# Kernel tuning notes

Hardware: AMD Instinct MI355X
Metric: run time of the kernel (lower is better)

The kernel has to match this reference:

```python
import jax, jax.numpy as jnp
import numpy as np

B, S, D = 8, 4096, 1536
NUM_ORGANISMS = 4
OUT = 2048


def setup_inputs() -> dict:
    key = jax.random.key(0)
    k_x, k_idx, k_w = jax.random.split(key, 3)
    x = jax.random.normal(k_x, (B, S, D), dtype=jnp.float32)
    organism_index = jax.random.randint(k_idx, (B,), 0, NUM_ORGANISMS, dtype=jnp.int32)
    # TruncatedNormal(stddev=1/sqrt(D)) init; plain normal*stddev is a faithful stand-in
    stddev = 1.0 / np.sqrt(D)
    w = jax.random.normal(k_w, (NUM_ORGANISMS, D, OUT), dtype=jnp.float32) * stddev
    b = jnp.zeros((NUM_ORGANISMS, OUT), dtype=jnp.float32)
    return {"x": x, "organism_index": organism_index, "w": w, "b": b}


def reference(x, organism_index, w, b):
    # Gather per-batch organism weights/biases (hard routing), then batched matmul.
    w_b = w[organism_index]          # [B, D, OUT]
    b_b = b[organism_index]          # [B, OUT]
    out = jnp.einsum('bsi,bij->bsj', x, w_b,
                     preferred_element_type=jnp.float32)  # [B, S, OUT]
    return out + b_b[:, None, :]
```

## Files before the change

kernel.cpp:

```cpp
#include <hip/hip_runtime.h>
#include <hip/hip_bf16.h>
#include <stdint.h>

#define B_    8
#define S_    4096
#define D_    1536
#define ORG_  4
#define OUT_  2048

typedef __bf16 bf16;
typedef __attribute__((ext_vector_type(8))) bf16  bf16x8;
typedef __attribute__((ext_vector_type(4))) float f32x4;

#define BK64 64
#define NKT  (D_ / BK64)

__global__ void k_cvt_x(const float* __restrict__ x, bf16* __restrict__ xb, long n8) {
  long i = (long)blockIdx.x * blockDim.x + threadIdx.x;
  long stride = (long)gridDim.x * blockDim.x;
  for (; i < n8; i += stride) {
    const float4* p = (const float4*)(x + i * 8);
    float4 a = p[0];
    float4 b = p[1];
    bf16x8 v;
    v[0] = (bf16)a.x; v[1] = (bf16)a.y; v[2] = (bf16)a.z; v[3] = (bf16)a.w;
    v[4] = (bf16)b.x; v[5] = (bf16)b.y; v[6] = (bf16)b.z; v[7] = (bf16)b.w;
    *(bf16x8*)(xb + i * 8) = v;
  }
}

__global__ void k_cvt_wT(const float* __restrict__ w, bf16* __restrict__ wt) {
  __shared__ float tile[32][33];
  int org = blockIdx.z;
  int n0 = blockIdx.x * 32;
  int d0 = blockIdx.y * 32;
  const float* wsrc = w + (size_t)org * D_ * OUT_;
  bf16* wdst = wt + (size_t)org * OUT_ * D_;
  int tx = threadIdx.x, ty = threadIdx.y;
#pragma unroll
  for (int j = 0; j < 32; j += 8)
    tile[ty + j][tx] = wsrc[(size_t)(d0 + ty + j) * OUT_ + (n0 + tx)];
  __syncthreads();
#pragma unroll
  for (int j = 0; j < 32; j += 8)
    wdst[(size_t)(n0 + ty + j) * D_ + (d0 + tx)] = (bf16)tile[tx][ty + j];
}

__global__ __launch_bounds__(512, 2)
void k_gemm256(const bf16* __restrict__ xb, const bf16* __restrict__ wt,
               const int* __restrict__ oidx, const float* __restrict__ bias,
               float* __restrict__ out) {
  __shared__ __align__(16) char smem[131072];
  char* const ldsA = smem;
  char* const ldsB = smem + 65536;

  const int batch = blockIdx.y;
  const int bx = blockIdx.x;
  const int swz = (bx & 7) * 16 + (bx >> 3);
  const int tn = swz >> 4, tm = swz & 15;
  const int m0 = tm * 256, n0 = tn * 256;
  const int org = oidx[batch];

  const bf16* Ag = xb + (size_t)batch * S_ * D_ + (size_t)m0 * D_;
  const bf16* Bg = wt + (size_t)org * OUT_ * D_ + (size_t)n0 * D_;

  const int tid  = threadIdx.x;
  const int lane = tid & 63, wv = tid >> 6;
  const int wr = wv >> 2, wc = wv & 3;
  const int lm = lane & 15, lk = lane >> 4;

  const int xo0 = (lk * 16) ^ ((lm & 7) << 4);
  const int xo1 = (64 + lk * 16) ^ ((lm & 7) << 4);
  const int arow = (wr * 128 + lm) * 128;
  const int brow = (wc * 64  + lm) * 128;

  const int srow = tid >> 3;
  const int scol = ((tid & 7) ^ ((tid >> 3) & 7)) << 3;
  const int soff = wv * 1024;

#define LDA(v, mi, kk) (*(const bf16x8*)(ldsA + (v)*32768 + arow + (mi)*2048 + ((kk) ? xo1 : xo0)))
#define LDB(v, ni, kk) (*(const bf16x8*)(ldsB + (v)*32768 + brow + (ni)*2048 + ((kk) ? xo1 : xo0)))

#define STAGE_HALF(gptr, ldsbase, h, kb) do {                                            \
    __builtin_amdgcn_global_load_lds(                                                    \
      (__attribute__((address_space(1))) void*)((gptr) + (size_t)((h)*128 + srow) * D_ + (kb) + scol), \
      (__attribute__((address_space(3))) void*)((ldsbase) + (h)*16384 + soff), 16, 0, 0);\
    __builtin_amdgcn_global_load_lds(                                                    \
      (__attribute__((address_space(1))) void*)((gptr) + (size_t)((h)*128 + 64 + srow) * D_ + (kb) + scol), \
      (__attribute__((address_space(3))) void*)((ldsbase) + (h)*16384 + 8192 + soff), 16, 0, 0); \
  } while (0)

#define SBAR()  __builtin_amdgcn_s_barrier()
#define LGK0()  asm volatile("s_waitcnt lgkmcnt(0)" ::: "memory")
#define VMC4()  asm volatile("s_waitcnt vmcnt(4)" ::: "memory")
#define VMC0()  asm volatile("s_waitcnt vmcnt(0)" ::: "memory")
#define PRIO(p) __builtin_amdgcn_s_setprio(p)

  bf16x8 a[4][2], b0[2][2], b1[2][2];
  f32x4 acc[8][4];
#pragma unroll
  for (int m = 0; m < 8; ++m)
#pragma unroll
    for (int n = 0; n < 4; ++n) acc[m][n] = (f32x4){0.f, 0.f, 0.f, 0.f};

#define READ_A(v, mb) do { _Pragma("unroll") for (int m = 0; m < 4; ++m) { \
    a[m][0] = LDA(v, (mb) + m, 0); a[m][1] = LDA(v, (mb) + m, 1); } } while (0)
#define READ_B(v, nb, bb) do { _Pragma("unroll") for (int n = 0; n < 2; ++n) { \
    bb[n][0] = LDB(v, (nb) + n, 0); bb[n][1] = LDB(v, (nb) + n, 1); } } while (0)
#define MFMA_Q(mb, nb, bb) do { \
    _Pragma("unroll") for (int m = 0; m < 4; ++m) \
    _Pragma("unroll") for (int n = 0; n < 2; ++n) \
    _Pragma("unroll") for (int kk = 0; kk < 2; ++kk) \
      acc[(mb)+m][(nb)+n] = __builtin_amdgcn_mfma_f32_16x16x32_bf16( \
          a[m][kk], bb[n][kk], acc[(mb)+m][(nb)+n], 0, 0, 0); } while (0)

  STAGE_HALF(Bg, ldsB, 0, 0);
  STAGE_HALF(Bg, ldsB, 1, 0);
  STAGE_HALF(Ag, ldsA, 0, 0);
  STAGE_HALF(Ag, ldsA, 1, 0);
  STAGE_HALF(Bg, ldsB + 32768, 0, BK64);
  STAGE_HALF(Bg, ldsB + 32768, 1, BK64);
  VMC4();
  SBAR();

  for (int i = 0; i < NKT / 2; ++i) {
    const int k1 = (2 * i + 1) * BK64;
    int t2 = 2 * i + 2; if (t2 > NKT - 1) t2 = NKT - 1;
    int t3 = 2 * i + 3; if (t3 > NKT - 1) t3 = NKT - 1;
    const int k2 = t2 * BK64, k3 = t3 * BK64;

    READ_A(0, 0); READ_B(0, 0, b0);
    STAGE_HALF(Ag, ldsA + 32768, 0, k1);
    SBAR(); LGK0();
    PRIO(1); MFMA_Q(0, 0, b0); PRIO(0);
    SBAR();
    READ_B(0, 2, b1);
    STAGE_HALF(Ag, ldsA + 32768, 1, k1);
    SBAR(); LGK0();
    PRIO(1); MFMA_Q(0, 2, b1); PRIO(0);
    SBAR();
    READ_A(0, 4);
    STAGE_HALF(Bg, ldsB, 0, k2);
    SBAR(); LGK0();
    PRIO(1); MFMA_Q(4, 0, b0); PRIO(0);
    SBAR();
    STAGE_HALF(Bg, ldsB, 1, k2);
    SBAR();
    PRIO(1); MFMA_Q(4, 2, b1); PRIO(0);
    VMC4();
    SBAR();
    READ_A(1, 0); READ_B(1, 0, b0);
    STAGE_HALF(Ag, ldsA, 0, k2);
    SBAR(); LGK0();
    PRIO(1); MFMA_Q(0, 0, b0); PRIO(0);
    SBAR();
    READ_B(1, 2, b1);
    STAGE_HALF(Ag, ldsA, 1, k2);
    SBAR(); LGK0();
    PRIO(1); MFMA_Q(0, 2, b1); PRIO(0);
    SBAR();
    READ_A(1, 4);
    STAGE_HALF(Bg, ldsB + 32768, 0, k3);
    SBAR(); LGK0();
    PRIO(1); MFMA_Q(4, 0, b0); PRIO(0);
    SBAR();
    STAGE_HALF(Bg, ldsB + 32768, 1, k3);
    SBAR();
    PRIO(1); MFMA_Q(4, 2, b1); PRIO(0);
    VMC4();
    SBAR();
  }

  VMC0();

  float* Og = out + (size_t)batch * S_ * OUT_ + (size_t)m0 * OUT_ + n0;
  const float* bbase = bias + (size_t)org * OUT_ + n0;
#pragma unroll
  for (int n = 0; n < 4; ++n) {
    const int col = wc * 64 + n * 16 + lm;
    const float bv = bbase[col];
#pragma unroll
    for (int m = 0; m < 8; ++m) {
#pragma unroll
      for (int r = 0; r < 4; ++r) {
        const int row = wr * 128 + m * 16 + lk * 4 + r;
        Og[(size_t)row * OUT_ + col] = acc[m][n][r] + bv;
      }
    }
  }
#undef LDA
#undef LDB
#undef STAGE_HALF
#undef SBAR
#undef LGK0
#undef VMC4
#undef VMC0
#undef PRIO
#undef READ_A
#undef READ_B
#undef MFMA_Q
}

__global__ void k_gemm_fallback(const float* __restrict__ x, const int* __restrict__ oidx,
                                const float* __restrict__ w, const float* __restrict__ bias,
                                float* __restrict__ out) {
  const int b = blockIdx.z;
  const int org = oidx[b];
  const int n = blockIdx.x * 64 + threadIdx.x;
  const int m = blockIdx.y * 4 + threadIdx.y;
  const float* xr = x + ((size_t)b * S_ + m) * D_;
  const float* wp = w + (size_t)org * D_ * OUT_ + n;
  float acc = 0.f;
  for (int k = 0; k < D_; ++k) acc += xr[k] * wp[(size_t)k * OUT_];
  out[((size_t)b * S_ + m) * OUT_ + n] = acc + bias[(size_t)org * OUT_ + n];
}

extern "C" void kernel_launch(void* const* d_in, const int* in_sizes, int n_in,
                              void* d_out, int out_size, void* d_ws, size_t ws_size,
                              hipStream_t stream) {
  const float* x    = (const float*)d_in[0];
  const int*   oidx = (const int*)d_in[1];
  const float* w    = (const float*)d_in[2];
  const float* bias = (const float*)d_in[3];
  float* out = (float*)d_out;

  const size_t xb_elems = (size_t)B_ * S_ * D_;
  const size_t wt_elems = (size_t)ORG_ * OUT_ * D_;
  const size_t need = (xb_elems + wt_elems) * sizeof(bf16);

  if (ws_size < need) {
    dim3 g(OUT_ / 64, S_ / 4, B_);
    k_gemm_fallback<<<g, dim3(64, 4), 0, stream>>>(x, oidx, w, bias, out);
    return;
  }

  bf16* xb = (bf16*)d_ws;
  bf16* wt = xb + xb_elems;

  k_cvt_x<<<2048, 256, 0, stream>>>(x, xb, (long)(xb_elems / 8));
  dim3 gt(OUT_ / 32, D_ / 32, ORG_);
  k_cvt_wT<<<gt, dim3(32, 8), 0, stream>>>(w, wt);
  dim3 gg(128, B_);
  k_gemm256<<<gg, 512, 0, stream>>>(xb, wt, oidx, bias, out);
}
```

Baseline: 313.2 us.

## Make GEMM persistent over four tiles with cross-tile prefetch

```diff
diff --git a/kernel.cpp b/kernel.cpp
--- a/kernel.cpp
+++ b/kernel.cpp
@@ -14,6 +14,7 @@
 
 #define BK64 64
 #define NKT  (D_ / BK64)
+#define ROUNDS 4
 
 __global__ void k_cvt_x(const float* __restrict__ x, bf16* __restrict__ xb, long n8) {
   long i = (long)blockIdx.x * blockDim.x + threadIdx.x;
@@ -47,22 +48,30 @@
 }
 
 __global__ __launch_bounds__(512, 2)
-void k_gemm256(const bf16* __restrict__ xb, const bf16* __restrict__ wt,
-               const int* __restrict__ oidx, const float* __restrict__ bias,
-               float* __restrict__ out) {
+void k_gemm_pers(const bf16* __restrict__ xb, const bf16* __restrict__ wt,
+                 const int* __restrict__ oidx, const float* __restrict__ bias,
+                 float* __restrict__ out) {
   __shared__ __align__(16) char smem[131072];
   char* const ldsA = smem;
   char* const ldsB = smem + 65536;
 
-  const int batch = blockIdx.y;
   const int bx = blockIdx.x;
-  const int swz = (bx & 7) * 16 + (bx >> 3);
-  const int tn = swz >> 4, tm = swz & 15;
-  const int m0 = tm * 256, n0 = tn * 256;
-  const int org = oidx[batch];
-
-  const bf16* Ag = xb + (size_t)batch * S_ * D_ + (size_t)m0 * D_;
-  const bf16* Bg = wt + (size_t)org * OUT_ * D_ + (size_t)n0 * D_;
+  const int gbase = (bx & 7) * 32 + (bx >> 3);
+
+  const bf16* AgR[ROUNDS]; const bf16* BgR[ROUNDS];
+  float* OgR[ROUNDS]; const float* bbR[ROUNDS];
+#pragma unroll
+  for (int r = 0; r < ROUNDS; ++r) {
+    const int G = gbase + r * 256;
+    const int pair = G >> 4, tm = G & 15;
+    const int batch = pair >> 3, tn = pair & 7;
+    const int m0 = tm * 256, n0 = tn * 256;
+    const int org = oidx[batch];
+    AgR[r] = xb + (size_t)batch * S_ * D_ + (size_t)m0 * D_;
+    BgR[r] = wt + (size_t)org * OUT_ * D_ + (size_t)n0 * D_;
+    OgR[r] = out + (size_t)batch * S_ * OUT_ + (size_t)m0 * OUT_ + n0;
+    bbR[r] = bias + (size_t)org * OUT_ + n0;
+  }
 
   const int tid  = threadIdx.x;
   const int lane = tid & 63, wv = tid >> 6;
@@ -92,6 +101,7 @@
 
 #define SBAR()  __builtin_amdgcn_s_barrier()
 #define LGK0()  asm volatile("s_waitcnt lgkmcnt(0)" ::: "memory")
+#define LGK8()  asm volatile("s_waitcnt lgkmcnt(8)" ::: "memory")
 #define VMC4()  asm volatile("s_waitcnt vmcnt(4)" ::: "memory")
 #define VMC0()  asm volatile("s_waitcnt vmcnt(0)" ::: "memory")
 #define PRIO(p) __builtin_amdgcn_s_setprio(p)
@@ -114,91 +124,108 @@
       acc[(mb)+m][(nb)+n] = __builtin_amdgcn_mfma_f32_16x16x32_bf16( \
           a[m][kk], bb[n][kk], acc[(mb)+m][(nb)+n], 0, 0, 0); } while (0)
 
-  STAGE_HALF(Bg, ldsB, 0, 0);
-  STAGE_HALF(Bg, ldsB, 1, 0);
-  STAGE_HALF(Ag, ldsA, 0, 0);
-  STAGE_HALF(Ag, ldsA, 1, 0);
-  STAGE_HALF(Bg, ldsB + 32768, 0, BK64);
-  STAGE_HALF(Bg, ldsB + 32768, 1, BK64);
+#define EPILOGUE(OgP, bbP) do { \
+    float* Og_ = (OgP); const float* bb_ = (bbP); \
+    _Pragma("unroll") for (int n = 0; n < 4; ++n) { \
+      const int col = wc * 64 + n * 16 + lm; \
+      const float bv = bb_[col]; \
+      _Pragma("unroll") for (int m = 0; m < 8; ++m) \
+      _Pragma("unroll") for (int rr = 0; rr < 4; ++rr) { \
+        const int row = wr * 128 + m * 16 + lk * 4 + rr; \
+        Og_[(size_t)row * OUT_ + col] = acc[m][n][rr] + bv; \
+      } \
+    } \
+    _Pragma("unroll") for (int m = 0; m < 8; ++m) \
+    _Pragma("unroll") for (int n = 0; n < 4; ++n) acc[m][n] = (f32x4){0.f, 0.f, 0.f, 0.f}; \
+  } while (0)
+
+  STAGE_HALF(BgR[0], ldsB, 0, 0);
+  STAGE_HALF(BgR[0], ldsB, 1, 0);
+  STAGE_HALF(AgR[0], ldsA, 0, 0);
+  STAGE_HALF(AgR[0], ldsA, 1, 0);
+  STAGE_HALF(BgR[0], ldsB + 32768, 0, BK64);
+  STAGE_HALF(BgR[0], ldsB + 32768, 1, BK64);
   VMC4();
   SBAR();
 
-  for (int i = 0; i < NKT / 2; ++i) {
-    const int k1 = (2 * i + 1) * BK64;
-    int t2 = 2 * i + 2; if (t2 > NKT - 1) t2 = NKT - 1;
-    int t3 = 2 * i + 3; if (t3 > NKT - 1) t3 = NKT - 1;
-    const int k2 = t2 * BK64, k3 = t3 * BK64;
-
-    READ_A(0, 0); READ_B(0, 0, b0);
-    STAGE_HALF(Ag, ldsA + 32768, 0, k1);
-    SBAR(); LGK0();
-    PRIO(1); MFMA_Q(0, 0, b0); PRIO(0);
-    SBAR();
-    READ_B(0, 2, b1);
-    STAGE_HALF(Ag, ldsA + 32768, 1, k1);
-    SBAR(); LGK0();
-    PRIO(1); MFMA_Q(0, 2, b1); PRIO(0);
-    SBAR();
-    READ_A(0, 4);
-    STAGE_HALF(Bg, ldsB, 0, k2);
-    SBAR(); LGK0();
-    PRIO(1); MFMA_Q(4, 0, b0); PRIO(0);
-    SBAR();
-    STAGE_HALF(Bg, ldsB, 1, k2);
-    SBAR();
-    PRIO(1); MFMA_Q(4, 2, b1); PRIO(0);
-    VMC4();
-    SBAR();
-    READ_A(1, 0); READ_B(1, 0, b0);
-    STAGE_HALF(Ag, ldsA, 0, k2);
-    SBAR(); LGK0();
-    PRIO(1); MFMA_Q(0, 0, b0); PRIO(0);
-    SBAR();
-    READ_B(1, 2, b1);
-    STAGE_HALF(Ag, ldsA, 1, k2);
-    SBAR(); LGK0();
-    PRIO(1); MFMA_Q(0, 2, b1); PRIO(0);
-    SBAR();
-    READ_A(1, 4);
-    STAGE_HALF(Bg, ldsB + 32768, 0, k3);
-    SBAR(); LGK0();
-    PRIO(1); MFMA_Q(4, 0, b0); PRIO(0);
-    SBAR();
-    STAGE_HALF(Bg, ldsB + 32768, 1, k3);
-    SBAR();
-    PRIO(1); MFMA_Q(4, 2, b1); PRIO(0);
-    VMC4();
-    SBAR();
-  }
-
-  VMC0();
-
-  float* Og = out + (size_t)batch * S_ * OUT_ + (size_t)m0 * OUT_ + n0;
-  const float* bbase = bias + (size_t)org * OUT_ + n0;
-#pragma unroll
-  for (int n = 0; n < 4; ++n) {
-    const int col = wc * 64 + n * 16 + lm;
-    const float bv = bbase[col];
-#pragma unroll
-    for (int m = 0; m < 8; ++m) {
-#pragma unroll
-      for (int r = 0; r < 4; ++r) {
-        const int row = wr * 128 + m * 16 + lk * 4 + r;
-        Og[(size_t)row * OUT_ + col] = acc[m][n][r] + bv;
-      }
+#pragma unroll
+  for (int r = 0; r < ROUNDS; ++r) {
+    const bf16* const AgCur = AgR[r];
+    const bf16* const BgCur = BgR[r];
+    const bf16* const AgNxt = AgR[r < ROUNDS - 1 ? r + 1 : ROUNDS - 1];
+    const bf16* const BgNxt = BgR[r < ROUNDS - 1 ? r + 1 : ROUNDS - 1];
+    const bool last = (r == ROUNDS - 1);
+
+    for (int j = 0; j < NKT / 2; ++j) {
+      const int k1 = (2 * j + 1) * BK64;
+      const bool cross = (j == NKT / 2 - 1);
+      const bf16* const A2 = cross ? AgNxt : AgCur;
+      const bf16* const B2 = cross ? BgNxt : BgCur;
+      const bf16* const B3 = cross ? BgNxt : BgCur;
+      const int k2 = cross ? (last ? (NKT - 1) * BK64 : 0) : (2 * j + 2) * BK64;
+      const int k3 = cross ? (last ? (NKT - 1) * BK64 : BK64) : (2 * j + 3) * BK64;
+
+      READ_A(0, 0); READ_B(0, 0, b0);
+      STAGE_HALF(AgCur, ldsA + 32768, 0, k1);
+      LGK8();
+      SBAR(); LGK0();
+      PRIO(1); MFMA_Q(0, 0, b0); PRIO(0);
+      SBAR();
+      READ_B(0, 2, b1);
+      STAGE_HALF(AgCur, ldsA + 32768, 1, k1);
+      SBAR(); LGK0();
+      PRIO(1); MFMA_Q(0, 2, b1); PRIO(0);
+      SBAR();
+      READ_A(0, 4);
+      STAGE_HALF(B2, ldsB, 0, k2);
+      SBAR(); LGK0();
+      PRIO(1); MFMA_Q(4, 0, b0); PRIO(0);
+      SBAR();
+      STAGE_HALF(B2, ldsB, 1, k2);
+      SBAR();
+      PRIO(1); MFMA_Q(4, 2, b1); PRIO(0);
+      VMC4();
+      SBAR();
+      READ_A(1, 0); READ_B(1, 0, b0);
+      STAGE_HALF(A2, ldsA, 0, k2);
+      LGK8();
+      SBAR(); LGK0();
+      PRIO(1); MFMA_Q(0, 0, b0); PRIO(0);
+      SBAR();
+      READ_B(1, 2, b1);
+      STAGE_HALF(A2, ldsA, 1, k2);
+      SBAR(); LGK0();
+      PRIO(1); MFMA_Q(0, 2, b1); PRIO(0);
+      SBAR();
+      READ_A(1, 4);
+      STAGE_HALF(B3, ldsB + 32768, 0, k3);
+      SBAR(); LGK0();
+      PRIO(1); MFMA_Q(4, 0, b0); PRIO(0);
+      SBAR();
+      STAGE_HALF(B3, ldsB + 32768, 1, k3);
+      SBAR();
+      PRIO(1); MFMA_Q(4, 2, b1); PRIO(0);
+      VMC4();
+      SBAR();
     }
-  }
+
+    if (last) VMC0();
+    EPILOGUE(OgR[r], bbR[r]);
+  }
+
 #undef LDA
 #undef LDB
 #undef STAGE_HALF
 #undef SBAR
 #undef LGK0
+#undef LGK8
 #undef VMC4
 #undef VMC0
 #undef PRIO
 #undef READ_A
 #undef READ_B
 #undef MFMA_Q
+#undef EPILOGUE
 }
 
 __global__ void k_gemm_fallback(const float* __restrict__ x, const int* __restrict__ oidx,
@@ -240,6 +267,5 @@
   k_cvt_x<<<2048, 256, 0, stream>>>(x, xb, (long)(xb_elems / 8));
   dim3 gt(OUT_ / 32, D_ / 32, ORG_);
   k_cvt_wT<<<gt, dim3(32, 8), 0, stream>>>(w, wt);
-  dim3 gg(128, B_);
-  k_gemm256<<<gg, 512, 0, stream>>>(xb, wt, oidx, bias, out);
-}
+  k_gemm_pers<<<256, 512, 0, stream>>>(xb, wt, oidx, bias, out);
+}
```

Result: slower. 490.1 us (+56.5%).
